# Performance work log

Hardware: AMD Instinct MI355X
Metric: run time of the kernel (lower is better)

The kernel has to match this reference:

```python
import jax, jax.numpy as jnp
import numpy as np

N, E = 50000, 800000
IN_DIM, OUT_DIM, H = 256, 128, 8
GEO_HID = 16  # RBF feature dim and geo_mlp hidden dim


def setup_inputs() -> dict:
    key = jax.random.key(0)
    ks = jax.random.split(key, 16)
    def lin(k, fan_out, fan_in):
        kw, kb = jax.random.split(k)
        lim = 1.0 / np.sqrt(fan_in)
        W = jax.random.uniform(kw, (fan_out, fan_in), jnp.float32, -lim, lim)
        b = jax.random.uniform(kb, (fan_out,), jnp.float32, -lim, lim)
        return W, b
    Wq, bq = lin(ks[0], OUT_DIM, IN_DIM)
    Wk, bk = lin(ks[1], OUT_DIM, IN_DIM)
    Wv, bv = lin(ks[2], OUT_DIM, IN_DIM)
    Wo, bo = lin(ks[3], OUT_DIM, OUT_DIM)
    Wg1, bg1 = lin(ks[4], GEO_HID, GEO_HID)
    Wg2, bg2 = lin(ks[5], H, GEO_HID)
    x = jax.random.normal(ks[6], (N, IN_DIM), jnp.float32)
    edge_index = jax.random.randint(ks[7], (2, E), 0, N, jnp.int64)
    edge_dist = jax.random.uniform(ks[8], (E,), jnp.float32) * 6.0
    return {"x": x, "edge_index": edge_index, "edge_dist": edge_dist,
            "Wq": Wq, "bq": bq, "Wk": Wk, "bk": bk, "Wv": Wv, "bv": bv,
            "Wo": Wo, "bo": bo, "Wg1": Wg1, "bg1": bg1, "Wg2": Wg2, "bg2": bg2}


def reference(x, edge_index, edge_dist, Wq, bq, Wk, bk, Wv, bv, Wo, bo, Wg1, bg1, Wg2, bg2):
    n = x.shape[0]
    num_heads = Wg2.shape[0]
    head_dim = Wq.shape[0] // num_heads
    scale = 1.0 / (head_dim ** 0.5)

    q = (x @ Wq.T + bq).reshape(n, num_heads, head_dim)
    k = (x @ Wk.T + bk).reshape(n, num_heads, head_dim)
    v = (x @ Wv.T + bv).reshape(n, num_heads, head_dim)

    # RBF expansion: 16 centers in [0, 6], gamma = 1.0
    centers = jnp.linspace(0.0, 6.0, GEO_HID)
    rbf = jnp.exp(-(edge_dist[:, None] - centers) ** 2)          # [E, 16]
    geo_bias = jax.nn.relu(rbf @ Wg1.T + bg1) @ Wg2.T + bg2      # [E, H]

    row, col = edge_index[0], edge_index[1]
    attn = (q[row] * k[col]).sum(-1) * scale + geo_bias          # [E, H]

    # segment softmax over incoming edges per destination node (row)
    m = jax.ops.segment_max(attn, row, num_segments=n)           # [N, H]
    e = jnp.exp(attn - m[row])
    s = jax.ops.segment_sum(e, row, num_segments=n)              # [N, H]
    a = e / (s[row] + 1e-12)                                     # [E, H]

    out = jax.ops.segment_sum(v[col] * a[:, :, None], row, num_segments=n)
    out = out.reshape(n, num_heads * head_dim)
    return out @ Wo.T + bo
```

## Files before the change

kernel.cpp:

```cpp
#include <hip/hip_runtime.h>
#include <math.h>

#define IN_DIM 256
#define OUT_DIM 128
#define NH 8
#define HD 16
#define GH 16
#define TBL 1024
#define LOG2E 1.44269504f
#define RCAP 64
#define BCAP 2560

typedef __attribute__((ext_vector_type(8))) short short8;
typedef __attribute__((ext_vector_type(4))) float floatx4;

__device__ __forceinline__ unsigned short f2bf(float f) {
    union { float f; unsigned u; } v; v.f = f;
    unsigned r = v.u + 0x7fffu + ((v.u >> 16) & 1u);
    return (unsigned short)(r >> 16);
}
__device__ __forceinline__ float bf2f(unsigned short h) {
    union { unsigned u; float f; } v; v.u = ((unsigned)h) << 16;
    return v.f;
}
__device__ __forceinline__ void split1(float f, unsigned short& h, unsigned short& l) {
    h = f2bf(f);
    l = f2bf(f - bf2f(h));
}
__device__ __forceinline__ float bflo(unsigned u) { return __uint_as_float(u << 16); }
__device__ __forceinline__ float bfhi(unsigned u) { return __uint_as_float(u & 0xffff0000u); }

__global__ __launch_bounds__(256) void prep_all_kernel(
    const float* __restrict__ x, const float* __restrict__ Wq, const float* __restrict__ Wk,
    const float* __restrict__ Wv, const float* __restrict__ Wo,
    unsigned short* __restrict__ xh, unsigned short* __restrict__ xl,
    unsigned short* __restrict__ wh, unsigned short* __restrict__ wl,
    unsigned short* __restrict__ wo_h, unsigned short* __restrict__ wo_l,
    const float* __restrict__ Wg1, const float* __restrict__ bg1,
    const float* __restrict__ Wg2, const float* __restrict__ bg2,
    float* __restrict__ tbl, int* __restrict__ gbin,
    int n4x, int nbins, int nsplit, int nwm, int nwo, int ngeo) {
    int bx = blockIdx.x;
    int t = threadIdx.x;

    if (bx < nsplit) {
        int i = bx * 256 + t;
        if (i >= n4x) return;
        float4 f = ((const float4*)x)[i];
        ushort4 h, l;
        split1(f.x, h.x, l.x); split1(f.y, h.y, l.y);
        split1(f.z, h.z, l.z); split1(f.w, h.w, l.w);
        ((ushort4*)xh)[i] = h;
        ((ushort4*)xl)[i] = l;
        return;
    }
    bx -= nsplit;
    if (bx < 3 * nwm) {
        int m = bx / nwm;
        int i = (bx - m * nwm) * 256 + t;
        if (i >= (OUT_DIM * IN_DIM) / 4) return;
        const float* W = (m == 0) ? Wq : (m == 1) ? Wk : Wv;
        float4 f = ((const float4*)W)[i];
        ushort4 h, l;
        split1(f.x, h.x, l.x); split1(f.y, h.y, l.y);
        split1(f.z, h.z, l.z); split1(f.w, h.w, l.w);
        size_t base = (size_t)m * (OUT_DIM * IN_DIM) / 4;
        ((ushort4*)wh)[base + i] = h;
        ((ushort4*)wl)[base + i] = l;
        return;
    }
    bx -= 3 * nwm;
    if (bx < nwo) {
        int i = bx * 256 + t;
        if (i >= (OUT_DIM * OUT_DIM) / 4) return;
        float4 f = ((const float4*)Wo)[i];
        ushort4 h, l;
        split1(f.x, h.x, l.x); split1(f.y, h.y, l.y);
        split1(f.z, h.z, l.z); split1(f.w, h.w, l.w);
        ((ushort4*)wo_h)[i] = h;
        ((ushort4*)wo_l)[i] = l;
        return;
    }
    bx -= nwo;
    if (bx < ngeo) {
        int i = bx * 256 + t;
        if (i >= TBL) return;
        float d = (float)i * (6.0f / (float)(TBL - 1));
        float rbf[GH];
#pragma unroll
        for (int j = 0; j < GH; ++j) {
            float c = 0.4f * (float)j;
            float tt = d - c;
            rbf[j] = __expf(-tt * tt);
        }
        float hid[GH];
#pragma unroll
        for (int j = 0; j < GH; ++j) {
            float acc = bg1[j];
#pragma unroll
            for (int kk = 0; kk < GH; ++kk) acc += rbf[kk] * Wg1[j * GH + kk];
            hid[j] = fmaxf(acc, 0.0f);
        }
#pragma unroll
        for (int h = 0; h < NH; ++h) {
            float acc = bg2[h];
#pragma unroll
            for (int j = 0; j < GH; ++j) acc += hid[j] * Wg2[h * GH + j];
            tbl[i * NH + h] = acc * LOG2E;
        }
        return;
    }
    for (int i = t; i < nbins; i += 256) gbin[i] = 0;
}

__global__ __launch_bounds__(256) void qkv_kernel(
    const unsigned short* __restrict__ xh, const unsigned short* __restrict__ xl,
    const unsigned short* __restrict__ wh, const unsigned short* __restrict__ wl,
    const float* __restrict__ bq, const float* __restrict__ bk, const float* __restrict__ bv,
    float* __restrict__ q, unsigned short* __restrict__ kb, unsigned short* __restrict__ vb,
    const int* __restrict__ ei, const float* __restrict__ edist,
    int* __restrict__ gbin, int2* __restrict__ binbuf,
    int Nn, int E_, int nxb, int nb1, int nbins) {
    __shared__ unsigned short xh_s[128 * 40];
    __shared__ unsigned short xl_s[128 * 40];
    __shared__ unsigned short wh_s[128 * 40];
    __shared__ unsigned short wl_s[128 * 40];

    const int tid = threadIdx.x;
    int bx = blockIdx.x;

    if (bx < nb1) {
        int* hist = (int*)xh_s;
        const int e0 = bx * 4096;
        for (int b = tid; b < nbins; b += 256) hist[b] = 0;
        __syncthreads();
#pragma unroll
        for (int i = 0; i < 16; ++i) {
            int e = e0 + tid + i * 256;
            if (e < E_) atomicAdd(&hist[ei[e] >> 7], 1);
        }
        __syncthreads();
        for (int b = tid; b < nbins; b += 256) {
            int h = hist[b];
            int base = 0;
            if (h) base = atomicAdd(&gbin[b], h);
            hist[b] = base;
        }
        __syncthreads();
#pragma unroll
        for (int i = 0; i < 16; ++i) {
            int e = e0 + tid + i * 256;
            if (e < E_) {
                int row = ei[e];
                int bin = row >> 7;
                int r = atomicAdd(&hist[bin], 1);
                float u = edist[e] * ((float)(TBL - 1) / 6.0f);
                u = fminf(fmaxf(u, 0.0f), (float)(TBL - 1));
                if (r < BCAP)
                    binbuf[(size_t)bin * BCAP + r] =
                        make_int2((ei[E_ + e] & 0x1FFFF) | ((row & 127) << 17), __float_as_int(u));
            }
        }
        return;
    }
    bx -= nb1;

    const int wsel = bx / nxb;
    const int n0 = (bx - wsel * nxb) * 128;
    const unsigned short* W_h = wh + (size_t)wsel * (OUT_DIM * IN_DIM);
    const unsigned short* W_l = wl + (size_t)wsel * (OUT_DIM * IN_DIM);
    const float* bias = (wsel == 0) ? bq : (wsel == 1) ? bk : bv;
    const bool vpath = (wsel == 2);

    const int w = tid >> 6;
    const int lane = tid & 63;
    const int ml = lane & 15;
    const int quad = lane >> 4;

    const int rows_valid = min(128, Nn - n0);

    floatx4 acc[2][8];
#pragma unroll
    for (int rr = 0; rr < 2; ++rr)
#pragma unroll
        for (int ct = 0; ct < 8; ++ct) acc[rr][ct] = (floatx4){0.f, 0.f, 0.f, 0.f};

    const short8 zero8 = {0, 0, 0, 0, 0, 0, 0, 0};

    for (int kc = 0; kc < IN_DIM; kc += 32) {
#pragma unroll
        for (int l = 0; l < 2; ++l) {
            int flat = tid + l * 256;
            int r = flat >> 2, c = flat & 3;
            size_t gx = (size_t)(n0 + r) * IN_DIM + kc + c * 8;
            size_t gw = (size_t)r * IN_DIM + kc + c * 8;
            short8 vh = zero8;
            if (r < rows_valid) vh = *(const short8*)(xh + gx);
            *(short8*)(xh_s + r * 40 + c * 8) = vh;
            *(short8*)(wh_s + r * 40 + c * 8) = *(const short8*)(W_h + gw);
            if (vpath) {
                short8 vl = zero8;
                if (r < rows_valid) vl = *(const short8*)(xl + gx);
                *(short8*)(xl_s + r * 40 + c * 8) = vl;
                *(short8*)(wl_s + r * 40 + c * 8) = *(const short8*)(W_l + gw);
            }
        }
        __syncthreads();

        short8 ah0 = *(const short8*)(xh_s + (w * 32 + ml) * 40 + quad * 8);
        short8 ah1 = *(const short8*)(xh_s + (w * 32 + 16 + ml) * 40 + quad * 8);
        if (!vpath) {
#pragma unroll
            for (int ct = 0; ct < 8; ++ct) {
                short8 bh = *(const short8*)(wh_s + (ct * 16 + ml) * 40 + quad * 8);
                acc[0][ct] = __builtin_amdgcn_mfma_f32_16x16x32_bf16(ah0, bh, acc[0][ct], 0, 0, 0);
                acc[1][ct] = __builtin_amdgcn_mfma_f32_16x16x32_bf16(ah1, bh, acc[1][ct], 0, 0, 0);
            }
        } else {
            short8 al0 = *(const short8*)(xl_s + (w * 32 + ml) * 40 + quad * 8);
            short8 al1 = *(const short8*)(xl_s + (w * 32 + 16 + ml) * 40 + quad * 8);
#pragma unroll
            for (int ct = 0; ct < 8; ++ct) {
                short8 bh = *(const short8*)(wh_s + (ct * 16 + ml) * 40 + quad * 8);
                short8 bl = *(const short8*)(wl_s + (ct * 16 + ml) * 40 + quad * 8);
                acc[0][ct] = __builtin_amdgcn_mfma_f32_16x16x32_bf16(ah0, bh, acc[0][ct], 0, 0, 0);
                acc[0][ct] = __builtin_amdgcn_mfma_f32_16x16x32_bf16(al0, bh, acc[0][ct], 0, 0, 0);
                acc[0][ct] = __builtin_amdgcn_mfma_f32_16x16x32_bf16(ah0, bl, acc[0][ct], 0, 0, 0);
                acc[1][ct] = __builtin_amdgcn_mfma_f32_16x16x32_bf16(ah1, bh, acc[1][ct], 0, 0, 0);
                acc[1][ct] = __builtin_amdgcn_mfma_f32_16x16x32_bf16(al1, bh, acc[1][ct], 0, 0, 0);
                acc[1][ct] = __builtin_amdgcn_mfma_f32_16x16x32_bf16(ah1, bl, acc[1][ct], 0, 0, 0);
            }
        }
        __syncthreads();
    }

    if (wsel == 0) {
#pragma unroll
        for (int rr = 0; rr < 2; ++rr)
#pragma unroll
            for (int ct = 0; ct < 8; ++ct) {
                float bj = bias[ct * 16 + ml];
#pragma unroll
                for (int r = 0; r < 4; ++r) {
                    int grow = n0 + w * 32 + rr * 16 + quad * 4 + r;
                    if (grow < Nn) q[(size_t)grow * 128 + ct * 16 + ml] = acc[rr][ct][r] + bj;
                }
            }
    } else {
        unsigned short* ob = (wsel == 1) ? kb : vb;
#pragma unroll
        for (int rr = 0; rr < 2; ++rr)
#pragma unroll
            for (int ct = 0; ct < 8; ++ct) {
                float bj = bias[ct * 16 + ml];
#pragma unroll
                for (int r = 0; r < 4; ++r) {
                    int grow = n0 + w * 32 + rr * 16 + quad * 4 + r;
                    if (grow < Nn) ob[(size_t)grow * 128 + ct * 16 + ml] = f2bf(acc[rr][ct][r] + bj);
                }
            }
    }
}

__global__ __launch_bounds__(256) void bin2bucket_kernel(
    const int2* __restrict__ binbuf, const int* __restrict__ gbin,
    int2* __restrict__ bucket, int* __restrict__ cnt, int Nn) {
    __shared__ int rcnt[128];
    const int bin = blockIdx.x;
    const int t = threadIdx.x;
    if (t < 128) rcnt[t] = 0;
    __syncthreads();
    int nb = gbin[bin];
    if (nb > BCAP) nb = BCAP;
    const int row0 = bin << 7;
    for (int i = t; i < nb; i += 256) {
        int2 p = binbuf[(size_t)bin * BCAP + i];
        int rowrel = (p.x >> 17) & 127;
        int col = p.x & 0x1FFFF;
        int r = atomicAdd(&rcnt[rowrel], 1);
        if (r < RCAP) bucket[(size_t)(row0 + rowrel) * RCAP + r] = make_int2(col, p.y);
    }
    __syncthreads();
    if (t < 128 && row0 + t < Nn) cnt[row0 + t] = min(rcnt[t], RCAP);
}

__global__ __launch_bounds__(256) void fused_node_kernel(
    const float* __restrict__ q, const unsigned short* __restrict__ kb,
    const unsigned short* __restrict__ vb, const int2* __restrict__ bucket,
    const float* __restrict__ tbl, const int* __restrict__ cnt,
    float* __restrict__ o, int Nn) {
    int lane = threadIdx.x & 63;
    int n = blockIdx.x * 4 + (threadIdx.x >> 6);
    if (n >= Nn) return;
    int g = lane >> 3;
    int h = lane & 7;
    int dcnt = cnt[n];
    int start = n * RCAP;
    int end = start + dcnt;

    float qf[16];
    {
        const float4* qp = (const float4*)(q + (size_t)n * 128 + h * 16);
#pragma unroll
        for (int j = 0; j < 4; ++j) {
            float4 t = qp[j];
            qf[j * 4 + 0] = t.x; qf[j * 4 + 1] = t.y;
            qf[j * 4 + 2] = t.z; qf[j * 4 + 3] = t.w;
        }
    }

    float l = 0.0f;
    float acc[16];
#pragma unroll
    for (int j = 0; j < 16; ++j) acc[j] = 0.0f;

#pragma unroll 2
    for (int base = start; base < end; base += 8) {
        int e = base + g;
        bool valid = (e < end);
        int ee = valid ? e : (end - 1);
        int2 np = bucket[ee];
        int col = np.x;
        float u = __int_as_float(np.y);

        const uint4* kp = (const uint4*)(kb + (size_t)col * 128 + h * 16);
        uint4 k0 = kp[0], k1 = kp[1];
        const uint4* vp = (const uint4*)(vb + (size_t)col * 128 + h * 16);
        uint4 v0 = vp[0], v1 = vp[1];

        unsigned kk[8] = {k0.x, k0.y, k0.z, k0.w, k1.x, k1.y, k1.z, k1.w};
        float d = 0.0f;
#pragma unroll
        for (int j = 0; j < 8; ++j) {
            d = fmaf(bflo(kk[j]), qf[2 * j], d);
            d = fmaf(bfhi(kk[j]), qf[2 * j + 1], d);
        }

        int i0 = min((int)u, TBL - 2);
        float fr = u - (float)i0;
        float t0 = tbl[i0 * NH + h];
        float t1 = tbl[i0 * NH + NH + h];
        float logit2 = fmaf(d, 0.25f * LOG2E, fmaf(fr, t1 - t0, t0));
        logit2 = fminf(logit2, 80.0f);
        if (!valid) logit2 = -1e30f;
        float p = __builtin_amdgcn_exp2f(logit2);

        l += p;
        unsigned vv[8] = {v0.x, v0.y, v0.z, v0.w, v1.x, v1.y, v1.z, v1.w};
#pragma unroll
        for (int j = 0; j < 8; ++j) {
            acc[2 * j]     = fmaf(p, bflo(vv[j]), acc[2 * j]);
            acc[2 * j + 1] = fmaf(p, bfhi(vv[j]), acc[2 * j + 1]);
        }
    }

#pragma unroll
    for (int off = 8; off < 64; off <<= 1) {
        l += __shfl_xor(l, off);
#pragma unroll
        for (int j = 0; j < 16; ++j) acc[j] += __shfl_xor(acc[j], off);
    }

    if (g == 0) {
        float inv = 1.0f / (l + 1e-12f);
        float4* op = (float4*)(o + (size_t)n * 128 + h * 16);
#pragma unroll
        for (int j = 0; j < 4; ++j) {
            float4 t;
            t.x = acc[j * 4 + 0] * inv; t.y = acc[j * 4 + 1] * inv;
            t.z = acc[j * 4 + 2] * inv; t.w = acc[j * 4 + 3] * inv;
            op[j] = t;
        }
    }
}

__global__ __launch_bounds__(256) void out_gemm_mfma_kernel(
    const float* __restrict__ o,
    const unsigned short* __restrict__ wo_h, const unsigned short* __restrict__ wo_l,
    const float* __restrict__ bo, float* __restrict__ out, int Nn) {
    const int n0 = blockIdx.x * 64;

    __shared__ unsigned short xh_s[64 * 40];
    __shared__ unsigned short xl_s[64 * 40];
    __shared__ unsigned short wh_s[128 * 40];
    __shared__ unsigned short wl_s[128 * 40];

    const int tid = threadIdx.x;
    const int w = tid >> 6;
    const int lane = tid & 63;
    const int ml = lane & 15;
    const int quad = lane >> 4;

    const int rows_valid = min(64, Nn - n0);

    floatx4 acc[8];
#pragma unroll
    for (int ct = 0; ct < 8; ++ct) acc[ct] = (floatx4){0.f, 0.f, 0.f, 0.f};

    for (int kc = 0; kc < OUT_DIM; kc += 32) {
        {
            int r = tid >> 2, c = tid & 3;
            unsigned short hv[8], lv[8];
            if (r < rows_valid) {
                const float* src = o + (size_t)(n0 + r) * OUT_DIM + kc + c * 8;
#pragma unroll
                for (int j = 0; j < 8; ++j) split1(src[j], hv[j], lv[j]);
            } else {
#pragma unroll
                for (int j = 0; j < 8; ++j) { hv[j] = 0; lv[j] = 0; }
            }
            *(short8*)(xh_s + r * 40 + c * 8) = *(short8*)hv;
            *(short8*)(xl_s + r * 40 + c * 8) = *(short8*)lv;
        }
#pragma unroll
        for (int l = 0; l < 2; ++l) {
            int idx = tid + l * 256;
            int r = idx >> 2, c = idx & 3;
            size_t g = (size_t)r * OUT_DIM + kc + c * 8;
            *(short8*)(wh_s + r * 40 + c * 8) = *(const short8*)(wo_h + g);
            *(short8*)(wl_s + r * 40 + c * 8) = *(const short8*)(wo_l + g);
        }
        __syncthreads();

        short8 ah = *(const short8*)(xh_s + (w * 16 + ml) * 40 + quad * 8);
        short8 al = *(const short8*)(xl_s + (w * 16 + ml) * 40 + quad * 8);
#pragma unroll
        for (int ct = 0; ct < 8; ++ct) {
            short8 bh = *(const short8*)(wh_s + (ct * 16 + ml) * 40 + quad * 8);
            short8 bl = *(const short8*)(wl_s + (ct * 16 + ml) * 40 + quad * 8);
            acc[ct] = __builtin_amdgcn_mfma_f32_16x16x32_bf16(ah, bh, acc[ct], 0, 0, 0);
            acc[ct] = __builtin_amdgcn_mfma_f32_16x16x32_bf16(al, bh, acc[ct], 0, 0, 0);
            acc[ct] = __builtin_amdgcn_mfma_f32_16x16x32_bf16(ah, bl, acc[ct], 0, 0, 0);
        }
        __syncthreads();
    }

#pragma unroll
    for (int ct = 0; ct < 8; ++ct) {
        float bj = bo[ct * 16 + ml];
#pragma unroll
        for (int r = 0; r < 4; ++r) {
            int grow = n0 + w * 16 + quad * 4 + r;
            if (grow < Nn) out[(size_t)grow * 128 + ct * 16 + ml] = acc[ct][r] + bj;
        }
    }
}

extern "C" void kernel_launch(void* const* d_in, const int* in_sizes, int n_in,
                              void* d_out, int out_size, void* d_ws, size_t ws_size,
                              hipStream_t stream) {
    const float* x   = (const float*)d_in[0];
    const int* ei    = (const int*)d_in[1];
    const float* edist = (const float*)d_in[2];
    const float* Wq = (const float*)d_in[3];  const float* bq = (const float*)d_in[4];
    const float* Wk = (const float*)d_in[5];  const float* bk = (const float*)d_in[6];
    const float* Wv = (const float*)d_in[7];  const float* bv = (const float*)d_in[8];
    const float* Wo = (const float*)d_in[9];  const float* bo = (const float*)d_in[10];
    const float* Wg1 = (const float*)d_in[11]; const float* bg1 = (const float*)d_in[12];
    const float* Wg2 = (const float*)d_in[13]; const float* bg2 = (const float*)d_in[14];
    const int Nn = in_sizes[0] / IN_DIM;
    const int Ee = in_sizes[2];
    float* out = (float*)d_out;

    char* ws = (char*)d_ws;
    size_t off = 0;
    auto alloc = [&](size_t bytes) -> char* {
        char* p = ws + off;
        off += (bytes + 255) & ~(size_t)255;
        return p;
    };
    float* q  = (float*)alloc((size_t)Nn * 128 * 4);
    unsigned short* kbuf = (unsigned short*)alloc((size_t)Nn * 128 * 2);
    unsigned short* vbuf = (unsigned short*)alloc((size_t)Nn * 128 * 2);
    char* xlblock = alloc((size_t)Nn * IN_DIM * 2);
    float* o = (float*)alloc((size_t)Nn * 128 * 4);
    float* geot = (float*)alloc((size_t)TBL * 8 * 4);
    int* cnt = (int*)alloc((size_t)Nn * 4);
    int nbins = (Nn + 127) >> 7;
    int* gbin = (int*)alloc((size_t)nbins * 4);
    unsigned short* wh_all = (unsigned short*)alloc((size_t)3 * OUT_DIM * IN_DIM * 2);
    unsigned short* wl_all = (unsigned short*)alloc((size_t)3 * OUT_DIM * IN_DIM * 2);
    unsigned short* wo_h = (unsigned short*)alloc((size_t)OUT_DIM * OUT_DIM * 2);
    unsigned short* wo_l = (unsigned short*)alloc((size_t)OUT_DIM * OUT_DIM * 2);
    int2* bucket = (int2*)alloc((size_t)Nn * RCAP * 8);

    int2* binbuf = (int2*)o;

    unsigned short* xh = (unsigned short*)d_out;
    unsigned short* xl = (unsigned short*)xlblock;

    int n4x = Nn * IN_DIM / 4;
    int nsplit = (n4x + 255) / 256;
    int nwm = ((OUT_DIM * IN_DIM / 4) + 255) / 256;
    int nwo = ((OUT_DIM * OUT_DIM / 4) + 255) / 256;
    int ngeo = (TBL + 255) / 256;
    int gprep = nsplit + 3 * nwm + nwo + ngeo + 1;
    prep_all_kernel<<<gprep, 256, 0, stream>>>(
        x, Wq, Wk, Wv, Wo, xh, xl, wh_all, wl_all, wo_h, wo_l,
        Wg1, bg1, Wg2, bg2, geot, gbin, n4x, nbins, nsplit, nwm, nwo, ngeo);

    int nxb = (Nn + 127) / 128;
    int nb1 = (Ee + 4095) / 4096;
    qkv_kernel<<<nb1 + 3 * nxb, 256, 0, stream>>>(
        xh, xl, wh_all, wl_all, bq, bk, bv, q, kbuf, vbuf,
        ei, edist, gbin, binbuf, Nn, Ee, nxb, nb1, nbins);

    bin2bucket_kernel<<<nbins, 256, 0, stream>>>(binbuf, gbin, bucket, cnt, Nn);

    fused_node_kernel<<<(Nn + 3) / 4, 256, 0, stream>>>(q, kbuf, vbuf, bucket, geot, cnt, o, Nn);

    out_gemm_mfma_kernel<<<(Nn + 63) / 64, 256, 0, stream>>>(o, wo_h, wo_l, bo, out, Nn);
}
```

Measured before the change: 289.3 us.

## Compact edge buckets in CSR form, prefetch edges, widen GEMM blocks to 512 threads

bin2bucket now stages each bin's edges in shared memory, prefix-sums the per-row counts and writes a compact CSR-like bucket with per-row start offsets, replacing the sparse padded Nn*64 layout. fused_node_kernel reads rowstart and software-prefetches the next edge pair. The qkv and output GEMM kernels move to 512-thread blocks with 2D warp tiling (4 row groups x 2 column groups), and the output GEMM tile grows to 128 rows. This cuts bucket memory footprint and scattered writes, and adds a shared-memory scan plus higher register and occupancy pressure in exchange.

```diff
diff --git a/kernel.cpp b/kernel.cpp
--- a/kernel.cpp
+++ b/kernel.cpp
@@ -113,7 +113,7 @@
     for (int i = t; i < nbins; i += 256) gbin[i] = 0;
 }
 
-__global__ __launch_bounds__(256) void qkv_kernel(
+__global__ __launch_bounds__(512, 4) void qkv_kernel(
     const unsigned short* __restrict__ xh, const unsigned short* __restrict__ xl,
     const unsigned short* __restrict__ wh, const unsigned short* __restrict__ wl,
     const float* __restrict__ bq, const float* __restrict__ bk, const float* __restrict__ bv,
@@ -132,15 +132,15 @@
     if (bx < nb1) {
         int* hist = (int*)xh_s;
         const int e0 = bx * 4096;
-        for (int b = tid; b < nbins; b += 256) hist[b] = 0;
-        __syncthreads();
-#pragma unroll
-        for (int i = 0; i < 16; ++i) {
-            int e = e0 + tid + i * 256;
+        for (int b = tid; b < nbins; b += 512) hist[b] = 0;
+        __syncthreads();
+#pragma unroll
+        for (int i = 0; i < 8; ++i) {
+            int e = e0 + tid + i * 512;
             if (e < E_) atomicAdd(&hist[ei[e] >> 7], 1);
         }
         __syncthreads();
-        for (int b = tid; b < nbins; b += 256) {
+        for (int b = tid; b < nbins; b += 512) {
             int h = hist[b];
             int base = 0;
             if (h) base = atomicAdd(&gbin[b], h);
@@ -148,8 +148,8 @@
         }
         __syncthreads();
 #pragma unroll
-        for (int i = 0; i < 16; ++i) {
-            int e = e0 + tid + i * 256;
+        for (int i = 0; i < 8; ++i) {
+            int e = e0 + tid + i * 512;
             if (e < E_) {
                 int row = ei[e];
                 int bin = row >> 7;
@@ -176,22 +176,22 @@
     const int lane = tid & 63;
     const int ml = lane & 15;
     const int quad = lane >> 4;
+    const int rg = w & 3;
+    const int cg = w >> 2;
 
     const int rows_valid = min(128, Nn - n0);
 
-    floatx4 acc[2][8];
+    floatx4 acc[2][4];
 #pragma unroll
     for (int rr = 0; rr < 2; ++rr)
 #pragma unroll
-        for (int ct = 0; ct < 8; ++ct) acc[rr][ct] = (floatx4){0.f, 0.f, 0.f, 0.f};
+        for (int ct = 0; ct < 4; ++ct) acc[rr][ct] = (floatx4){0.f, 0.f, 0.f, 0.f};
 
     const short8 zero8 = {0, 0, 0, 0, 0, 0, 0, 0};
 
     for (int kc = 0; kc < IN_DIM; kc += 32) {
-#pragma unroll
-        for (int l = 0; l < 2; ++l) {
-            int flat = tid + l * 256;
-            int r = flat >> 2, c = flat & 3;
+        {
+            int r = tid >> 2, c = tid & 3;
             size_t gx = (size_t)(n0 + r) * IN_DIM + kc + c * 8;
             size_t gw = (size_t)r * IN_DIM + kc + c * 8;
             short8 vh = zero8;
@@ -207,22 +207,22 @@
         }
         __syncthreads();
 
-        short8 ah0 = *(const short8*)(xh_s + (w * 32 + ml) * 40 + quad * 8);
-        short8 ah1 = *(const short8*)(xh_s + (w * 32 + 16 + ml) * 40 + quad * 8);
+        short8 ah0 = *(const short8*)(xh_s + (rg * 32 + ml) * 40 + quad * 8);
+        short8 ah1 = *(const short8*)(xh_s + (rg * 32 + 16 + ml) * 40 + quad * 8);
         if (!vpath) {
 #pragma unroll
-            for (int ct = 0; ct < 8; ++ct) {
-                short8 bh = *(const short8*)(wh_s + (ct * 16 + ml) * 40 + quad * 8);
+            for (int ct = 0; ct < 4; ++ct) {
+                short8 bh = *(const short8*)(wh_s + (cg * 64 + ct * 16 + ml) * 40 + quad * 8);
                 acc[0][ct] = __builtin_amdgcn_mfma_f32_16x16x32_bf16(ah0, bh, acc[0][ct], 0, 0, 0);
                 acc[1][ct] = __builtin_amdgcn_mfma_f32_16x16x32_bf16(ah1, bh, acc[1][ct], 0, 0, 0);
             }
         } else {
-            short8 al0 = *(const short8*)(xl_s + (w * 32 + ml) * 40 + quad * 8);
-            short8 al1 = *(const short8*)(xl_s + (w * 32 + 16 + ml) * 40 + quad * 8);
-#pragma unroll
-            for (int ct = 0; ct < 8; ++ct) {
-                short8 bh = *(const short8*)(wh_s + (ct * 16 + ml) * 40 + quad * 8);
-                short8 bl = *(const short8*)(wl_s + (ct * 16 + ml) * 40 + quad * 8);
+            short8 al0 = *(const short8*)(xl_s + (rg * 32 + ml) * 40 + quad * 8);
+            short8 al1 = *(const short8*)(xl_s + (rg * 32 + 16 + ml) * 40 + quad * 8);
+#pragma unroll
+            for (int ct = 0; ct < 4; ++ct) {
+                short8 bh = *(const short8*)(wh_s + (cg * 64 + ct * 16 + ml) * 40 + quad * 8);
+                short8 bl = *(const short8*)(wl_s + (cg * 64 + ct * 16 + ml) * 40 + quad * 8);
                 acc[0][ct] = __builtin_amdgcn_mfma_f32_16x16x32_bf16(ah0, bh, acc[0][ct], 0, 0, 0);
                 acc[0][ct] = __builtin_amdgcn_mfma_f32_16x16x32_bf16(al0, bh, acc[0][ct], 0, 0, 0);
                 acc[0][ct] = __builtin_amdgcn_mfma_f32_16x16x32_bf16(ah0, bl, acc[0][ct], 0, 0, 0);
@@ -238,12 +238,13 @@
 #pragma unroll
         for (int rr = 0; rr < 2; ++rr)
 #pragma unroll
-            for (int ct = 0; ct < 8; ++ct) {
-                float bj = bias[ct * 16 + ml];
+            for (int ct = 0; ct < 4; ++ct) {
+                int col = cg * 64 + ct * 16 + ml;
+                float bj = bias[col];
 #pragma unroll
                 for (int r = 0; r < 4; ++r) {
-                    int grow = n0 + w * 32 + rr * 16 + quad * 4 + r;
-                    if (grow < Nn) q[(size_t)grow * 128 + ct * 16 + ml] = acc[rr][ct][r] + bj;
+                    int grow = n0 + rg * 32 + rr * 16 + quad * 4 + r;
+                    if (grow < Nn) q[(size_t)grow * 128 + col] = acc[rr][ct][r] + bj;
                 }
             }
     } else {
@@ -251,12 +252,13 @@
 #pragma unroll
         for (int rr = 0; rr < 2; ++rr)
 #pragma unroll
-            for (int ct = 0; ct < 8; ++ct) {
-                float bj = bias[ct * 16 + ml];
+            for (int ct = 0; ct < 4; ++ct) {
+                int col = cg * 64 + ct * 16 + ml;
+                float bj = bias[col];
 #pragma unroll
                 for (int r = 0; r < 4; ++r) {
-                    int grow = n0 + w * 32 + rr * 16 + quad * 4 + r;
-                    if (grow < Nn) ob[(size_t)grow * 128 + ct * 16 + ml] = f2bf(acc[rr][ct][r] + bj);
+                    int grow = n0 + rg * 32 + rr * 16 + quad * 4 + r;
+                    if (grow < Nn) ob[(size_t)grow * 128 + col] = f2bf(acc[rr][ct][r] + bj);
                 }
             }
     }
@@ -264,8 +266,10 @@
 
 __global__ __launch_bounds__(256) void bin2bucket_kernel(
     const int2* __restrict__ binbuf, const int* __restrict__ gbin,
-    int2* __restrict__ bucket, int* __restrict__ cnt, int Nn) {
+    int2* __restrict__ bucket, int* __restrict__ rowstart, int* __restrict__ cnt, int Nn) {
     __shared__ int rcnt[128];
+    __shared__ int pref[128];
+    __shared__ int2 ebuf[BCAP];
     const int bin = blockIdx.x;
     const int t = threadIdx.x;
     if (t < 128) rcnt[t] = 0;
@@ -273,30 +277,61 @@
     int nb = gbin[bin];
     if (nb > BCAP) nb = BCAP;
     const int row0 = bin << 7;
-    for (int i = t; i < nb; i += 256) {
-        int2 p = binbuf[(size_t)bin * BCAP + i];
-        int rowrel = (p.x >> 17) & 127;
-        int col = p.x & 0x1FFFF;
-        int r = atomicAdd(&rcnt[rowrel], 1);
-        if (r < RCAP) bucket[(size_t)(row0 + rowrel) * RCAP + r] = make_int2(col, p.y);
+
+    int px[10], py[10], rk[10];
+#pragma unroll
+    for (int j = 0; j < 10; ++j) {
+        int i = t + j * 256;
+        rk[j] = -1;
+        if (i < nb) {
+            int2 p = binbuf[(size_t)bin * BCAP + i];
+            int rowrel = (p.x >> 17) & 127;
+            int r = atomicAdd(&rcnt[rowrel], 1);
+            if (r < RCAP) { px[j] = p.x & 0x1FFFF; py[j] = p.y; rk[j] = r | (rowrel << 16); }
+        }
     }
     __syncthreads();
-    if (t < 128 && row0 + t < Nn) cnt[row0 + t] = min(rcnt[t], RCAP);
+    int myclamp = 0;
+    if (t < 128) { myclamp = min(rcnt[t], RCAP); pref[t] = myclamp; }
+    __syncthreads();
+    for (int off = 1; off < 128; off <<= 1) {
+        int v = 0;
+        if (t < 128 && t >= off) v = pref[t - off];
+        __syncthreads();
+        if (t < 128) pref[t] += v;
+        __syncthreads();
+    }
+#pragma unroll
+    for (int j = 0; j < 10; ++j) {
+        if (rk[j] >= 0) {
+            int rowrel = rk[j] >> 16;
+            int r = rk[j] & 0xFFFF;
+            int pos = pref[rowrel] - min(rcnt[rowrel], RCAP) + r;
+            ebuf[pos] = make_int2(px[j], py[j]);
+        }
+    }
+    __syncthreads();
+    int total = pref[127];
+    const int obase = bin * BCAP;
+    for (int i = t; i < total; i += 256) bucket[obase + i] = ebuf[i];
+    if (t < 128 && row0 + t < Nn) {
+        rowstart[row0 + t] = obase + pref[t] - myclamp;
+        cnt[row0 + t] = myclamp;
+    }
 }
 
 __global__ __launch_bounds__(256) void fused_node_kernel(
     const float* __restrict__ q, const unsigned short* __restrict__ kb,
     const unsigned short* __restrict__ vb, const int2* __restrict__ bucket,
-    const float* __restrict__ tbl, const int* __restrict__ cnt,
+    const float* __restrict__ tbl, const int* __restrict__ rowstart, const int* __restrict__ cnt,
     float* __restrict__ o, int Nn) {
     int lane = threadIdx.x & 63;
     int n = blockIdx.x * 4 + (threadIdx.x >> 6);
     if (n >= Nn) return;
     int g = lane >> 3;
     int h = lane & 7;
-    int dcnt = cnt[n];
-    int start = n * RCAP;
-    int end = start + dcnt;
+    int start = rowstart[n];
+    int end = start + cnt[n];
 
     float qf[16];
     {
@@ -314,14 +349,18 @@
 #pragma unroll
     for (int j = 0; j < 16; ++j) acc[j] = 0.0f;
 
+    int2 np;
+    if (start < end) np = bucket[min(start + g, end - 1)];
+
 #pragma unroll 2
     for (int base = start; base < end; base += 8) {
-        int e = base + g;
-        bool valid = (e < end);
-        int ee = valid ? e : (end - 1);
-        int2 np = bucket[ee];
-        int col = np.x;
-        float u = __int_as_float(np.y);
+        bool valid = (base + g < end);
+        int2 cur = np;
+        int nxt = base + 8;
+        if (nxt < end) np = bucket[min(nxt + g, end - 1)];
+
+        int col = cur.x;
+        float u = __int_as_float(cur.y);
 
         const uint4* kp = (const uint4*)(kb + (size_t)col * 128 + h * 16);
         uint4 k0 = kp[0], k1 = kp[1];
@@ -374,14 +413,14 @@
     }
 }
 
-__global__ __launch_bounds__(256) void out_gemm_mfma_kernel(
+__global__ __launch_bounds__(512, 4) void out_gemm_mfma_kernel(
     const float* __restrict__ o,
     const unsigned short* __restrict__ wo_h, const unsigned short* __restrict__ wo_l,
     const float* __restrict__ bo, float* __restrict__ out, int Nn) {
-    const int n0 = blockIdx.x * 64;
-
-    __shared__ unsigned short xh_s[64 * 40];
-    __shared__ unsigned short xl_s[64 * 40];
+    const int n0 = blockIdx.x * 128;
+
+    __shared__ unsigned short xh_s[128 * 40];
+    __shared__ unsigned short xl_s[128 * 40];
     __shared__ unsigned short wh_s[128 * 40];
     __shared__ unsigned short wl_s[128 * 40];
 
@@ -390,12 +429,16 @@
     const int lane = tid & 63;
     const int ml = lane & 15;
     const int quad = lane >> 4;
-
-    const int rows_valid = min(64, Nn - n0);
-
-    floatx4 acc[8];
-#pragma unroll
-    for (int ct = 0; ct < 8; ++ct) acc[ct] = (floatx4){0.f, 0.f, 0.f, 0.f};
+    const int rg = w & 3;
+    const int cg = w >> 2;
+
+    const int rows_valid = min(128, Nn - n0);
+
+    floatx4 acc[2][4];
+#pragma unroll
+    for (int rr = 0; rr < 2; ++rr)
+#pragma unroll
+        for (int ct = 0; ct < 4; ++ct) acc[rr][ct] = (floatx4){0.f, 0.f, 0.f, 0.f};
 
     for (int kc = 0; kc < OUT_DIM; kc += 32) {
         {
@@ -411,39 +454,42 @@
             }
             *(short8*)(xh_s + r * 40 + c * 8) = *(short8*)hv;
             *(short8*)(xl_s + r * 40 + c * 8) = *(short8*)lv;
-        }
-#pragma unroll
-        for (int l = 0; l < 2; ++l) {
-            int idx = tid + l * 256;
-            int r = idx >> 2, c = idx & 3;
-            size_t g = (size_t)r * OUT_DIM + kc + c * 8;
-            *(short8*)(wh_s + r * 40 + c * 8) = *(const short8*)(wo_h + g);
-            *(short8*)(wl_s + r * 40 + c * 8) = *(const short8*)(wo_l + g);
-        }
-        __syncthreads();
-
-        short8 ah = *(const short8*)(xh_s + (w * 16 + ml) * 40 + quad * 8);
-        short8 al = *(const short8*)(xl_s + (w * 16 + ml) * 40 + quad * 8);
-#pragma unroll
-        for (int ct = 0; ct < 8; ++ct) {
-            short8 bh = *(const short8*)(wh_s + (ct * 16 + ml) * 40 + quad * 8);
-            short8 bl = *(const short8*)(wl_s + (ct * 16 + ml) * 40 + quad * 8);
-            acc[ct] = __builtin_amdgcn_mfma_f32_16x16x32_bf16(ah, bh, acc[ct], 0, 0, 0);
-            acc[ct] = __builtin_amdgcn_mfma_f32_16x16x32_bf16(al, bh, acc[ct], 0, 0, 0);
-            acc[ct] = __builtin_amdgcn_mfma_f32_16x16x32_bf16(ah, bl, acc[ct], 0, 0, 0);
-        }
-        __syncthreads();
-    }
-
-#pragma unroll
-    for (int ct = 0; ct < 8; ++ct) {
-        float bj = bo[ct * 16 + ml];
-#pragma unroll
-        for (int r = 0; r < 4; ++r) {
-            int grow = n0 + w * 16 + quad * 4 + r;
-            if (grow < Nn) out[(size_t)grow * 128 + ct * 16 + ml] = acc[ct][r] + bj;
-        }
-    }
+            size_t gg = (size_t)r * OUT_DIM + kc + c * 8;
+            *(short8*)(wh_s + r * 40 + c * 8) = *(const short8*)(wo_h + gg);
+            *(short8*)(wl_s + r * 40 + c * 8) = *(const short8*)(wo_l + gg);
+        }
+        __syncthreads();
+
+        short8 ah0 = *(const short8*)(xh_s + (rg * 32 + ml) * 40 + quad * 8);
+        short8 ah1 = *(const short8*)(xh_s + (rg * 32 + 16 + ml) * 40 + quad * 8);
+        short8 al0 = *(const short8*)(xl_s + (rg * 32 + ml) * 40 + quad * 8);
+        short8 al1 = *(const short8*)(xl_s + (rg * 32 + 16 + ml) * 40 + quad * 8);
+#pragma unroll
+        for (int ct = 0; ct < 4; ++ct) {
+            short8 bh = *(const short8*)(wh_s + (cg * 64 + ct * 16 + ml) * 40 + quad * 8);
+            short8 bl = *(const short8*)(wl_s + (cg * 64 + ct * 16 + ml) * 40 + quad * 8);
+            acc[0][ct] = __builtin_amdgcn_mfma_f32_16x16x32_bf16(ah0, bh, acc[0][ct], 0, 0, 0);
+            acc[0][ct] = __builtin_amdgcn_mfma_f32_16x16x32_bf16(al0, bh, acc[0][ct], 0, 0, 0);
+            acc[0][ct] = __builtin_amdgcn_mfma_f32_16x16x32_bf16(ah0, bl, acc[0][ct], 0, 0, 0);
+            acc[1][ct] = __builtin_amdgcn_mfma_f32_16x16x32_bf16(ah1, bh, acc[1][ct], 0, 0, 0);
+            acc[1][ct] = __builtin_amdgcn_mfma_f32_16x16x32_bf16(al1, bh, acc[1][ct], 0, 0, 0);
+            acc[1][ct] = __builtin_amdgcn_mfma_f32_16x16x32_bf16(ah1, bl, acc[1][ct], 0, 0, 0);
+        }
+        __syncthreads();
+    }
+
+#pragma unroll
+    for (int rr = 0; rr < 2; ++rr)
+#pragma unroll
+        for (int ct = 0; ct < 4; ++ct) {
+            int col = cg * 64 + ct * 16 + ml;
+            float bj = bo[col];
+#pragma unroll
+            for (int r = 0; r < 4; ++r) {
+                int grow = n0 + rg * 32 + rr * 16 + quad * 4 + r;
+                if (grow < Nn) out[(size_t)grow * 128 + col] = acc[rr][ct][r] + bj;
+            }
+        }
 }
 
 extern "C" void kernel_launch(void* const* d_in, const int* in_sizes, int n_in,
@@ -476,13 +522,14 @@
     float* o = (float*)alloc((size_t)Nn * 128 * 4);
     float* geot = (float*)alloc((size_t)TBL * 8 * 4);
     int* cnt = (int*)alloc((size_t)Nn * 4);
+    int* rowstart = (int*)alloc((size_t)Nn * 4);
     int nbins = (Nn + 127) >> 7;
     int* gbin = (int*)alloc((size_t)nbins * 4);
     unsigned short* wh_all = (unsigned short*)alloc((size_t)3 * OUT_DIM * IN_DIM * 2);
     unsigned short* wl_all = (unsigned short*)alloc((size_t)3 * OUT_DIM * IN_DIM * 2);
     unsigned short* wo_h = (unsigned short*)alloc((size_t)OUT_DIM * OUT_DIM * 2);
     unsigned short* wo_l = (unsigned short*)alloc((size_t)OUT_DIM * OUT_DIM * 2);
-    int2* bucket = (int2*)alloc((size_t)Nn * RCAP * 8);
+    int2* bucket = (int2*)alloc((size_t)nbins * BCAP * 8);
 
     int2* binbuf = (int2*)o;
 
@@ -501,13 +548,13 @@
 
     int nxb = (Nn + 127) / 128;
     int nb1 = (Ee + 4095) / 4096;
-    qkv_kernel<<<nb1 + 3 * nxb, 256, 0, stream>>>(
+    qkv_kernel<<<nb1 + 3 * nxb, 512, 0, stream>>>(
         xh, xl, wh_all, wl_all, bq, bk, bv, q, kbuf, vbuf,
         ei, edist, gbin, binbuf, Nn, Ee, nxb, nb1, nbins);
 
-    bin2bucket_kernel<<<nbins, 256, 0, stream>>>(binbuf, gbin, bucket, cnt, Nn);
-
-    fused_node_kernel<<<(Nn + 3) / 4, 256, 0, stream>>>(q, kbuf, vbuf, bucket, geot, cnt, o, Nn);
-
-    out_gemm_mfma_kernel<<<(Nn + 63) / 64, 256, 0, stream>>>(o, wo_h, wo_l, bo, out, Nn);
-}
+    bin2bucket_kernel<<<nbins, 256, 0, stream>>>(binbuf, gbin, bucket, rowstart, cnt, Nn);
+
+    fused_node_kernel<<<(Nn + 3) / 4, 256, 0, stream>>>(q, kbuf, vbuf, bucket, geot, rowstart, cnt, o, Nn);
+
+    out_gemm_mfma_kernel<<<(Nn + 127) / 128, 512, 0, stream>>>(o, wo_h, wo_l, bo, out, Nn);
+}
```

After: 270.7 us. -6.4%, faster.
